# Kernel optimization log

Hardware: AMD Instinct MI355X
Metric: run time of the kernel (lower is better)

Reference implementation:

```python
import jax, jax.numpy as jnp
import numpy as np

N = 100000   # nodes
E = 1600000  # edges (before self loops)
IN, HID, HEADS, OUT = 128, 32, 2, 32


def setup_inputs() -> dict:
    key = jax.random.key(0)
    ks = jax.random.split(key, 10)
    def glorot(k, shape, fan_in):
        return jax.random.normal(k, shape, dtype=jnp.float32) / np.sqrt(fan_in)
    return {
        "x": jax.random.normal(ks[0], (N, IN), dtype=jnp.float32),
        "edge_index": jax.random.randint(ks[1], (2, E), 0, N, dtype=jnp.int32),
        "W1": glorot(ks[2], (IN, HEADS * HID), IN),
        "a_src1": glorot(ks[3], (HEADS, HID), HID),
        "a_dst1": glorot(ks[4], (HEADS, HID), HID),
        "b1": jnp.zeros((HEADS * HID,), dtype=jnp.float32),
        "W2": glorot(ks[5], (HEADS * HID, OUT), HEADS * HID),
        "a_src2": glorot(ks[6], (1, OUT), OUT),
        "a_dst2": glorot(ks[7], (1, OUT), OUT),
        "b2": jnp.zeros((OUT,), dtype=jnp.float32),
    }


def gat_conv(x, W, a_src, a_dst, b, src, dst, n):
    """PyG-style GATConv: shared linear, edge softmax over incoming edges, sum aggregate."""
    H, C = a_src.shape
    xl = (x @ W).reshape(n, H, C)                       # [N, H, C]
    asn = jnp.einsum('nhc,hc->nh', xl, a_src)            # per-node source score
    adn = jnp.einsum('nhc,hc->nh', xl, a_dst)            # per-node dest score
    e = jax.nn.leaky_relu(asn[src] + adn[dst], 0.2)      # [E', H]
    m = jax.ops.segment_max(e, dst, num_segments=n)      # stable softmax per dest
    m = jnp.where(jnp.isfinite(m), m, 0.0)
    ex = jnp.exp(e - m[dst])
    denom = jax.ops.segment_sum(ex, dst, num_segments=n)
    alpha = ex / (denom[dst] + 1e-16)                    # [E', H]
    out = jax.ops.segment_sum(xl[src] * alpha[:, :, None], dst, num_segments=n)
    return out.reshape(n, H * C) + b


def reference(x, edge_index, W1, a_src1, a_dst1, b1, W2, a_src2, a_dst2, b2):
    n = x.shape[0]
    loop = jnp.arange(n, dtype=edge_index.dtype)         # add self loops (PyG default)
    src = jnp.concatenate([edge_index[0], loop])
    dst = jnp.concatenate([edge_index[1], loop])
    h = jax.nn.relu(gat_conv(x, W1, a_src1, a_dst1, b1, src, dst, n))
    # F.dropout(p=0.5) is identity in eval mode
    return gat_conv(h, W2, a_src2, a_dst2, b2, src, dst, n)
```

## Files before the change

kernel.cpp:

```cpp
#include <hip/hip_runtime.h>
#include <hip/hip_fp16.h>


#define BS 256
#define PCHUNK 8192
#define CAPB 5632
#define GPAD 16

typedef _Float16 half8 __attribute__((ext_vector_type(8)));
typedef float f32x4 __attribute__((ext_vector_type(4)));

__global__ __launch_bounds__(BS) void k_init(int* __restrict__ gcursor, int nbuk) {
    for (int i = threadIdx.x; i < nbuk; i += BS) gcursor[i * GPAD] = i * CAPB;
}

__global__ __launch_bounds__(BS) void k_pg1(const int* __restrict__ ei, int E, int n,
                                            int* __restrict__ gcursor, int* __restrict__ ppair,
                                            const float* __restrict__ x, const float* __restrict__ W,
                                            const float* __restrict__ asrc, const float* __restrict__ adst,
                                            signed char* __restrict__ xl, float* __restrict__ scA,
                                            float* __restrict__ scD, int gC) {
    __shared__ _Float16 smem[8192];
    int tid = threadIdx.x;
    if ((int)blockIdx.x < gC) {
        int* cnt  = (int*)smem;
        int* gpos = cnt + 512;
        int* lcur = cnt + 1024;
        cnt[tid] = 0; cnt[tid + 256] = 0;
        lcur[tid] = 0; lcur[tid + 256] = 0;
        __syncthreads();
        const int* dstp = ei + E;
        int base = blockIdx.x * PCHUNK;
        bool full = (base + PCHUNK <= E);
        if (full) {
            const int4* dv = (const int4*)(dstp + base) + tid * 8;
#pragma unroll
            for (int k = 0; k < 8; k++) {
                int4 d4 = dv[k];
                atomicAdd(&cnt[d4.x >> 8], 1);
                atomicAdd(&cnt[d4.y >> 8], 1);
                atomicAdd(&cnt[d4.z >> 8], 1);
                atomicAdd(&cnt[d4.w >> 8], 1);
            }
        } else {
            for (int i = tid; base + i < E; i += BS)
                atomicAdd(&cnt[dstp[base + i] >> 8], 1);
        }
        __syncthreads();
        for (int b = tid; b < 512; b += BS) {
            int c = cnt[b];
            if (c > 0) gpos[b] = atomicAdd(&gcursor[b * GPAD], c);
        }
        __syncthreads();
        if (full) {
            const int4* sv = (const int4*)(ei + base) + tid * 8;
            const int4* dv = (const int4*)(dstp + base) + tid * 8;
#pragma unroll 2
            for (int k = 0; k < 8; k++) {
                int4 s4 = sv[k];
                int4 d4 = dv[k];
                int d, s, b, r;
                d = d4.x; s = s4.x; b = d >> 8; r = atomicAdd(&lcur[b], 1);
                ppair[gpos[b] + r] = ((d & 255) << 17) | s;
                d = d4.y; s = s4.y; b = d >> 8; r = atomicAdd(&lcur[b], 1);
                ppair[gpos[b] + r] = ((d & 255) << 17) | s;
                d = d4.z; s = s4.z; b = d >> 8; r = atomicAdd(&lcur[b], 1);
                ppair[gpos[b] + r] = ((d & 255) << 17) | s;
                d = d4.w; s = s4.w; b = d >> 8; r = atomicAdd(&lcur[b], 1);
                ppair[gpos[b] + r] = ((d & 255) << 17) | s;
            }
        } else {
            for (int i = tid; base + i < E; i += BS) {
                int s = ei[base + i], d = dstp[base + i];
                int b = d >> 8;
                int r = atomicAdd(&lcur[b], 1);
                ppair[gpos[b] + r] = ((d & 255) << 17) | s;
            }
        }
        return;
    }
    _Float16* wf = smem;
#pragma unroll
    for (int v = 0; v < 8; v++) {
        int w = (v * 256 + tid) * 4;
        float4 ww = *(const float4*)(W + w);
        int k = w >> 6, c0 = w & 63;
        int kt = k >> 5, j = k & 7, lnh = (k >> 3) & 3;
        int nt = c0 >> 4;
        int f = kt * 4 + nt;
        int bidx = (f * 64 + lnh * 16 + (c0 & 15)) * 8 + j;
        wf[bidx]      = (_Float16)ww.x;
        wf[bidx + 8]  = (_Float16)ww.y;
        wf[bidx + 16] = (_Float16)ww.z;
        wf[bidx + 24] = (_Float16)ww.w;
    }
    __syncthreads();
    int wave = tid >> 6, lane = tid & 63;
    int nb = ((blockIdx.x - gC) * 4 + wave) * 16;
    int m = lane & 15, q = lane >> 4;
    int node_m = nb + m; if (node_m >= n) node_m = n - 1;
    half8 bf[4][4];
#pragma unroll
    for (int f = 0; f < 16; f++)
        bf[f >> 2][f & 3] = *(half8*)&wf[(f * 64 + lane) * 8];
    f32x4 acc[4] = {f32x4{0,0,0,0}, f32x4{0,0,0,0}, f32x4{0,0,0,0}, f32x4{0,0,0,0}};
#pragma unroll
    for (int kt = 0; kt < 4; kt++) {
        const float* xp = x + (size_t)node_m * 128 + kt * 32 + q * 8;
        float4 xa = *(const float4*)xp;
        float4 xb = *(const float4*)(xp + 4);
        half8 a;
        a[0] = (_Float16)xa.x; a[1] = (_Float16)xa.y; a[2] = (_Float16)xa.z; a[3] = (_Float16)xa.w;
        a[4] = (_Float16)xb.x; a[5] = (_Float16)xb.y; a[6] = (_Float16)xb.z; a[7] = (_Float16)xb.w;
#pragma unroll
        for (int nt = 0; nt < 4; nt++)
            acc[nt] = __builtin_amdgcn_mfma_f32_16x16x32_f16(a, bf[kt][nt], acc[nt], 0, 0, 0);
    }
    int c = lane & 15;
    float a_s[4], a_d[4];
#pragma unroll
    for (int nt = 0; nt < 4; nt++) { a_s[nt] = asrc[nt * 16 + c]; a_d[nt] = adst[nt * 16 + c]; }
#pragma unroll
    for (int r = 0; r < 4; r++) {
        int node = nb + q * 4 + r;
        bool ok = node < n;
        float v0 = acc[0][r], v1 = acc[1][r], v2 = acc[2][r], v3 = acc[3][r];
        float as0 = v0 * a_s[0] + v1 * a_s[1];
        float as1 = v2 * a_s[2] + v3 * a_s[3];
        float ad0 = v0 * a_d[0] + v1 * a_d[1];
        float ad1 = v2 * a_d[2] + v3 * a_d[3];
        float mxv = fmaxf(fmaxf(fabsf(v0), fabsf(v1)), fmaxf(fabsf(v2), fabsf(v3)));
#pragma unroll
        for (int off = 1; off < 16; off <<= 1) {
            as0 += __shfl_xor(as0, off); as1 += __shfl_xor(as1, off);
            ad0 += __shfl_xor(ad0, off); ad1 += __shfl_xor(ad1, off);
            mxv = fmaxf(mxv, __shfl_xor(mxv, off));
        }
        if (ok) {
            float inv = mxv > 1e-30f ? 127.f / mxv : 0.f;
            float scl = mxv * (1.f / 127.f);
            signed char* row = xl + (size_t)node * 64;
            row[c]      = (signed char)(int)rintf(v0 * inv);
            row[16 + c] = (signed char)(int)rintf(v1 * inv);
            row[32 + c] = (signed char)(int)rintf(v2 * inv);
            row[48 + c] = (signed char)(int)rintf(v3 * inv);
            if (c == 0) {
                ((float4*)scA)[node] = make_float4(as0, as1, scl, 0.f);
                ((float2*)scD)[node] = make_float2(ad0, ad1);
            }
        }
    }
}

__global__ __launch_bounds__(BS) void k_bucket(const int* __restrict__ ppair,
                                               const int* __restrict__ gcursor, int n,
                                               int* __restrict__ col,
                                               int* __restrict__ row_ptr, int* __restrict__ row_end) {
    __shared__ int ldeg[256];
    __shared__ int lscan[256];
    __shared__ int lcur[256];
    __shared__ int lcol[CAPB];
    int b = blockIdx.x;
    int t = threadIdx.x;
    int lo = b << 8;
    int hi = lo + 256; if (hi > n) hi = n;
    int W = hi - lo;
    int base = b * CAPB;
    int cnt = gcursor[b * GPAD] - base;
    if (cnt > CAPB) cnt = CAPB;
    ldeg[t] = 0;
    __syncthreads();
    for (int i = t; i < cnt; i += BS)
        atomicAdd(&ldeg[ppair[base + i] >> 17], 1);
    __syncthreads();
    lscan[t] = ldeg[t];
    __syncthreads();
    for (int off = 1; off < 256; off <<= 1) {
        int a = (t >= off) ? lscan[t - off] : 0;
        __syncthreads();
        lscan[t] += a;
        __syncthreads();
    }
    {
        int e0 = lscan[t] - ldeg[t];
        lcur[t] = e0;
        if (t < W) { row_ptr[lo + t] = base + e0; row_end[lo + t] = base + e0 + ldeg[t]; }
    }
    __syncthreads();
    for (int i = t; i < cnt; i += BS) {
        int p = ppair[base + i];
        int r = atomicAdd(&lcur[p >> 17], 1);
        if (r < CAPB) lcol[r] = p & 131071;
    }
    __syncthreads();
    for (int i = t; i < cnt; i += BS) col[base + i] = lcol[i];
}

__global__ __launch_bounds__(BS) void k_ag1g2(const int* __restrict__ row_ptr, const int* __restrict__ row_end,
                                              const int* __restrict__ col, const signed char* __restrict__ xl,
                                              const float* __restrict__ scA, const float* __restrict__ scD,
                                              const float* __restrict__ b1,
                                              const float* __restrict__ W2,
                                              const float* __restrict__ as2, const float* __restrict__ ad2,
                                              __half* __restrict__ xl2, float* __restrict__ sc2, int n) {
    __shared__ _Float16 hsh[32 * 72];
    __shared__ _Float16 wf2[2048];
    int tid = threadIdx.x;
#pragma unroll
    for (int v = 0; v < 2; v++) {
        int w = (v * 256 + tid) * 4;
        float4 ww = *(const float4*)(W2 + w);
        int k = w >> 5, c0 = w & 31;
        int kt = k >> 5, j = k & 7, lnh = (k >> 3) & 3;
        int nt = c0 >> 4;
        int f = kt * 2 + nt;
        int bidx = (f * 64 + lnh * 16 + (c0 & 15)) * 8 + j;
        wf2[bidx]      = (_Float16)ww.x;
        wf2[bidx + 8]  = (_Float16)ww.y;
        wf2[bidx + 16] = (_Float16)ww.z;
        wf2[bidx + 24] = (_Float16)ww.w;
    }
    int node_local = tid >> 3;
    int node = blockIdx.x * 32 + node_local;
    int tc = tid & 7;
    int lane = tid & 63;
    int tb = lane & 56;
    bool alive = node < n;
    int nodeC = alive ? node : n - 1;
    int s0 = row_ptr[nodeC], e1 = row_end[nodeC];
    float4 sA = ((const float4*)scA)[nodeC];
    float2 sD = ((const float2*)scD)[nodeC];
    bool hh0 = tc < 4;
    float adn = hh0 ? sD.x : sD.y;
    float es0 = sA.x + sD.x; es0 = fmaxf(es0, 0.2f * es0);
    float es1 = sA.y + sD.y; es1 = fmaxf(es1, 0.2f * es1);
    float xs = __expf(hh0 ? es0 : es1);
    uint2 rawS = *(const uint2*)(xl + (size_t)nodeC * 64 + tc * 8);
    float ws0 = xs * sA.z;
    int sx = (int)rawS.x, sy = (int)rawS.y;
    float acc0 = ws0 * (float)(signed char)(sx);
    float acc1 = ws0 * (float)(signed char)(sx >> 8);
    float acc2 = ws0 * (float)(signed char)(sx >> 16);
    float acc3 = ws0 * (float)(signed char)(sx >> 24);
    float acc4 = ws0 * (float)(signed char)(sy);
    float acc5 = ws0 * (float)(signed char)(sy >> 8);
    float acc6 = ws0 * (float)(signed char)(sy >> 16);
    float acc7 = ws0 * (float)(signed char)(sy >> 24);
    float den = xs;
    int deg = e1 - s0;
    int mx = deg;
    mx = max(mx, __shfl_xor(mx, 8));
    mx = max(mx, __shfl_xor(mx, 16));
    mx = max(mx, __shfl_xor(mx, 32));
    int nch = (mx + 7) >> 3;
    for (int ci = 0; ci < nch; ci++) {
        int pos = s0 + ci * 8;
        int m = e1 - pos; m = m < 0 ? 0 : (m > 8 ? 8 : m);
        int srcv = 0; float sgx = 0.f, sgy = 0.f, sgz = 0.f;
        if (tc < m) {
            srcv = col[pos + tc];
            float4 sg = ((const float4*)scA)[srcv];
            sgx = sg.x; sgy = sg.y; sgz = sg.z;
        }
#pragma unroll
        for (int kb = 0; kb < 8; kb += 4) {
            int rem = m - kb;
            if (rem > 0) {
                int nv = rem < 4 ? rem : 4;
                uint2 rr[4];
#pragma unroll
                for (int k = 0; k < 4; k++) {
                    if (k < nv) {
                        int sE = __shfl(srcv, tb + kb + k);
                        rr[k] = *(const uint2*)(xl + (size_t)sE * 64 + tc * 8);
                    }
                }
#pragma unroll
                for (int k = 0; k < 4; k++) {
                    if (k < nv) {
                        float a0 = __shfl(sgx, tb + kb + k);
                        float a1 = __shfl(sgy, tb + kb + k);
                        float sc_ = __shfl(sgz, tb + kb + k);
                        float as_ = hh0 ? a0 : a1;
                        float e = as_ + adn; e = fmaxf(e, 0.2f * e);
                        float w = __expf(e);
                        float wq = w * sc_;
                        int wx = (int)rr[k].x, wy = (int)rr[k].y;
                        acc0 = fmaf(wq, (float)(signed char)(wx), acc0);
                        acc1 = fmaf(wq, (float)(signed char)(wx >> 8), acc1);
                        acc2 = fmaf(wq, (float)(signed char)(wx >> 16), acc2);
                        acc3 = fmaf(wq, (float)(signed char)(wx >> 24), acc3);
                        acc4 = fmaf(wq, (float)(signed char)(wy), acc4);
                        acc5 = fmaf(wq, (float)(signed char)(wy >> 8), acc5);
                        acc6 = fmaf(wq, (float)(signed char)(wy >> 16), acc6);
                        acc7 = fmaf(wq, (float)(signed char)(wy >> 24), acc7);
                        den += w;
                    }
                }
            }
        }
    }
    float dinv = 1.f / (den + 1e-16f);
    {
        float4 bvA = ((const float4*)b1)[tc * 2];
        float4 bvB = ((const float4*)b1)[tc * 2 + 1];
        __half2 p0 = __floats2half2_rn(fmaxf(fmaf(acc0, dinv, bvA.x), 0.f),
                                       fmaxf(fmaf(acc1, dinv, bvA.y), 0.f));
        __half2 p1 = __floats2half2_rn(fmaxf(fmaf(acc2, dinv, bvA.z), 0.f),
                                       fmaxf(fmaf(acc3, dinv, bvA.w), 0.f));
        __half2 p2 = __floats2half2_rn(fmaxf(fmaf(acc4, dinv, bvB.x), 0.f),
                                       fmaxf(fmaf(acc5, dinv, bvB.y), 0.f));
        __half2 p3 = __floats2half2_rn(fmaxf(fmaf(acc6, dinv, bvB.z), 0.f),
                                       fmaxf(fmaf(acc7, dinv, bvB.w), 0.f));
        uint4 o;
        o.x = *(unsigned int*)&p0; o.y = *(unsigned int*)&p1;
        o.z = *(unsigned int*)&p2; o.w = *(unsigned int*)&p3;
        *(uint4*)&hsh[node_local * 72 + tc * 8] = o;
    }
    __syncthreads();
    int wave = tid >> 6;
    if (wave < 2) {
        int m2 = lane & 15, q2 = lane >> 4;
        int nl = wave * 16 + m2;
        half8 bf[2][2];
#pragma unroll
        for (int f = 0; f < 4; f++)
            bf[f >> 1][f & 1] = *(half8*)&wf2[(f * 64 + lane) * 8];
        f32x4 acc2g[2] = {f32x4{0,0,0,0}, f32x4{0,0,0,0}};
#pragma unroll
        for (int kt = 0; kt < 2; kt++) {
            half8 a = *(half8*)&hsh[nl * 72 + kt * 32 + q2 * 8];
#pragma unroll
            for (int nt = 0; nt < 2; nt++)
                acc2g[nt] = __builtin_amdgcn_mfma_f32_16x16x32_f16(a, bf[kt][nt], acc2g[nt], 0, 0, 0);
        }
        int c = lane & 15;
        float a_s[2], a_d[2];
#pragma unroll
        for (int nt = 0; nt < 2; nt++) { a_s[nt] = as2[nt * 16 + c]; a_d[nt] = ad2[nt * 16 + c]; }
#pragma unroll
        for (int r = 0; r < 4; r++) {
            int nl_r = wave * 16 + q2 * 4 + r;
            int node_r = blockIdx.x * 32 + nl_r;
            bool ok = node_r < n;
            float v0 = acc2g[0][r], v1 = acc2g[1][r];
            float as = v0 * a_s[0] + v1 * a_s[1];
            float ad = v0 * a_d[0] + v1 * a_d[1];
#pragma unroll
            for (int off = 1; off < 16; off <<= 1) {
                as += __shfl_xor(as, off); ad += __shfl_xor(ad, off);
            }
            if (ok) {
                __half* row = xl2 + (size_t)node_r * 32;
                row[c]      = __float2half(v0);
                row[16 + c] = __float2half(v1);
                if (c == 0) ((float2*)sc2)[node_r] = make_float2(as, ad);
            }
        }
    }
}

__global__ __launch_bounds__(BS) void k_agg2(const int* __restrict__ row_ptr, const int* __restrict__ row_end,
                                             const int* __restrict__ col, const __half* __restrict__ xl,
                                             const float* __restrict__ sc, const float* __restrict__ asrc,
                                             const float* __restrict__ b2,
                                             float* __restrict__ out, int n) {
    int tid = blockIdx.x * BS + threadIdx.x;
    int node = tid >> 2;
    int tc = threadIdx.x & 3;
    int lane = threadIdx.x & 63;
    int tb = lane & 60;
    bool alive = node < n;
    if (!alive) node = n - 1;
    int s0 = row_ptr[node], e1 = row_end[node];
    float2 sn = ((const float2*)sc)[node];
    float adn = sn.y;
    float es = sn.x + adn; es = fmaxf(es, 0.2f * es);
    float xs = __expf(es);
    uint4 rawS = *(const uint4*)(xl + (size_t)node * 32 + tc * 8);
    __half2 sh0 = *(__half2*)&rawS.x, sh1 = *(__half2*)&rawS.y;
    __half2 sh2 = *(__half2*)&rawS.z, sh3 = *(__half2*)&rawS.w;
    float acc0 = xs * __low2float(sh0), acc1 = xs * __high2float(sh0);
    float acc2 = xs * __low2float(sh1), acc3 = xs * __high2float(sh1);
    float acc4 = xs * __low2float(sh2), acc5 = xs * __high2float(sh2);
    float acc6 = xs * __low2float(sh3), acc7 = xs * __high2float(sh3);
    float den = xs;
    int deg = e1 - s0;
    int mx = deg;
    mx = max(mx, __shfl_xor(mx, 4));
    mx = max(mx, __shfl_xor(mx, 8));
    mx = max(mx, __shfl_xor(mx, 16));
    mx = max(mx, __shfl_xor(mx, 32));
    int nch = (mx + 3) >> 2;
    for (int ci = 0; ci < nch; ci++) {
        int pos = s0 + ci * 4;
        int m = e1 - pos; m = m < 0 ? 0 : (m > 4 ? 4 : m);
        int srcv = 0; float sA = 0.f;
        if (tc < m) {
            srcv = col[pos + tc];
            sA = sc[(size_t)srcv * 2];
        }
        if (m > 0) {
            uint4 rr[4];
#pragma unroll
            for (int k = 0; k < 4; k++) {
                if (k < m) {
                    int sE = __shfl(srcv, tb + k);
                    rr[k] = *(const uint4*)(xl + (size_t)sE * 32 + tc * 8);
                }
            }
#pragma unroll
            for (int k = 0; k < 4; k++) {
                if (k < m) {
                    float s = __shfl(sA, tb + k);
                    float e = s + adn; e = fmaxf(e, 0.2f * e);
                    float w = __expf(e);
                    __half2 q0 = *(__half2*)&rr[k].x, q1 = *(__half2*)&rr[k].y;
                    __half2 q2 = *(__half2*)&rr[k].z, q3 = *(__half2*)&rr[k].w;
                    acc0 = fmaf(w, __low2float(q0), acc0); acc1 = fmaf(w, __high2float(q0), acc1);
                    acc2 = fmaf(w, __low2float(q1), acc2); acc3 = fmaf(w, __high2float(q1), acc3);
                    acc4 = fmaf(w, __low2float(q2), acc4); acc5 = fmaf(w, __high2float(q2), acc5);
                    acc6 = fmaf(w, __low2float(q3), acc6); acc7 = fmaf(w, __high2float(q3), acc7);
                    den += w;
                }
            }
        }
    }
    float dinv = 1.f / (den + 1e-16f);
    if (alive) {
        float4 bvA = ((const float4*)b2)[tc * 2];
        float4 bvB = ((const float4*)b2)[tc * 2 + 1];
        float4 oA, oB;
        oA.x = fmaf(acc0, dinv, bvA.x);
        oA.y = fmaf(acc1, dinv, bvA.y);
        oA.z = fmaf(acc2, dinv, bvA.z);
        oA.w = fmaf(acc3, dinv, bvA.w);
        oB.x = fmaf(acc4, dinv, bvB.x);
        oB.y = fmaf(acc5, dinv, bvB.y);
        oB.z = fmaf(acc6, dinv, bvB.z);
        oB.w = fmaf(acc7, dinv, bvB.w);
        float4* orow = (float4*)(out + (size_t)node * 32);
        orow[tc * 2]     = oA;
        orow[tc * 2 + 1] = oB;
    }
}

extern "C" void kernel_launch(void* const* d_in, const int* in_sizes, int n_in,
                              void* d_out, int out_size, void* d_ws, size_t ws_size,
                              hipStream_t stream) {
    const float* x    = (const float*)d_in[0];
    const int*   ei   = (const int*)d_in[1];
    const float* W1   = (const float*)d_in[2];
    const float* as1  = (const float*)d_in[3];
    const float* ad1  = (const float*)d_in[4];
    const float* b1   = (const float*)d_in[5];
    const float* W2   = (const float*)d_in[6];
    const float* as2  = (const float*)d_in[7];
    const float* ad2  = (const float*)d_in[8];
    const float* b2   = (const float*)d_in[9];
    int n = in_sizes[0] / 128;
    int E = in_sizes[1] / 2;
    int NBUK = (n + 255) >> 8;

    char* w = (char*)d_ws;
    auto alloc = [&](size_t bytes) -> char* {
        char* p = w; w += (bytes + 255) / 256 * 256; return p;
    };
    int*    gcursor = (int*)alloc((size_t)NBUK * GPAD * 4);
    int*    ppair   = (int*)alloc((size_t)NBUK * CAPB * 4);
    int*    col     = (int*)alloc((size_t)NBUK * CAPB * 4);
    int*    row_ptr = (int*)alloc((size_t)n * 4);
    int*    row_end = (int*)alloc((size_t)n * 4);
    signed char* xl1 = (signed char*)alloc((size_t)n * 64);
    float*  scA     = (float*)alloc((size_t)n * 4 * 4);
    float*  scD     = (float*)alloc((size_t)n * 2 * 4);
    __half* xl2     = (__half*)alloc((size_t)n * 32 * 2);
    float*  sc2     = (float*)alloc((size_t)n * 2 * 4);

    int gC  = (E + PCHUNK - 1) / PCHUNK;
    int gG  = (n + 63) / 64;
    int gA1 = (n * 8 + BS - 1) / BS;
    int gA2 = (n * 4 + BS - 1) / BS;

    k_init   <<<1, BS, 0, stream>>>(gcursor, NBUK);
    k_pg1    <<<gC + gG, BS, 0, stream>>>(ei, E, n, gcursor, ppair,
                                          x, W1, as1, ad1, xl1, scA, scD, gC);
    k_bucket <<<NBUK, BS, 0, stream>>>(ppair, gcursor, n, col, row_ptr, row_end);
    k_ag1g2  <<<gA1, BS, 0, stream>>>(row_ptr, row_end, col, xl1, scA, scD, b1,
                                      W2, as2, ad2, xl2, sc2, n);
    k_agg2   <<<gA2, BS, 0, stream>>>(row_ptr, row_end, col, xl2, sc2, as2, b2,
                                      (float*)d_out, n);
}
```

Baseline: 211.3 us.

## Move layer-1 GEMM from partition kernel into bucket-sort kernel, 256 nodes per block

The layer-1 feature transform (x@W1 via MFMA, int8 quantization, attention scores) is taken out of the edge-partition kernel and fused into the per-bucket CSR build kernel as extra blocks. The partition kernel now runs alone with small shared memory, which should raise its occupancy. GEMM blocks now process 256 nodes each (4 tiles per wave), so W is converted to fp16 in LDS once per 256 nodes instead of once per 64. The catch is that the bucket kernel's large LDS footprint now also applies to the GEMM blocks, and the GEMM no longer overlaps with the atomic-heavy partition phase.

```diff
diff --git a/kernel.cpp b/kernel.cpp
--- a/kernel.cpp
+++ b/kernel.cpp
@@ -14,72 +14,118 @@
     for (int i = threadIdx.x; i < nbuk; i += BS) gcursor[i * GPAD] = i * CAPB;
 }
 
-__global__ __launch_bounds__(BS) void k_pg1(const int* __restrict__ ei, int E, int n,
-                                            int* __restrict__ gcursor, int* __restrict__ ppair,
-                                            const float* __restrict__ x, const float* __restrict__ W,
-                                            const float* __restrict__ asrc, const float* __restrict__ adst,
-                                            signed char* __restrict__ xl, float* __restrict__ scA,
-                                            float* __restrict__ scD, int gC) {
-    __shared__ _Float16 smem[8192];
+__global__ __launch_bounds__(BS) void k_part(const int* __restrict__ ei, int E, int n,
+                                             int* __restrict__ gcursor, int* __restrict__ ppair) {
+    __shared__ int smem[1536];
     int tid = threadIdx.x;
-    if ((int)blockIdx.x < gC) {
-        int* cnt  = (int*)smem;
-        int* gpos = cnt + 512;
-        int* lcur = cnt + 1024;
-        cnt[tid] = 0; cnt[tid + 256] = 0;
-        lcur[tid] = 0; lcur[tid + 256] = 0;
+    int* cnt  = smem;
+    int* gpos = cnt + 512;
+    int* lcur = cnt + 1024;
+    cnt[tid] = 0; cnt[tid + 256] = 0;
+    lcur[tid] = 0; lcur[tid + 256] = 0;
+    __syncthreads();
+    const int* dstp = ei + E;
+    int base = blockIdx.x * PCHUNK;
+    bool full = (base + PCHUNK <= E);
+    if (full) {
+        const int4* dv = (const int4*)(dstp + base) + tid * 8;
+#pragma unroll
+        for (int k = 0; k < 8; k++) {
+            int4 d4 = dv[k];
+            atomicAdd(&cnt[d4.x >> 8], 1);
+            atomicAdd(&cnt[d4.y >> 8], 1);
+            atomicAdd(&cnt[d4.z >> 8], 1);
+            atomicAdd(&cnt[d4.w >> 8], 1);
+        }
+    } else {
+        for (int i = tid; base + i < E; i += BS)
+            atomicAdd(&cnt[dstp[base + i] >> 8], 1);
+    }
+    __syncthreads();
+    for (int b = tid; b < 512; b += BS) {
+        int c = cnt[b];
+        if (c > 0) gpos[b] = atomicAdd(&gcursor[b * GPAD], c);
+    }
+    __syncthreads();
+    if (full) {
+        const int4* sv = (const int4*)(ei + base) + tid * 8;
+        const int4* dv = (const int4*)(dstp + base) + tid * 8;
+#pragma unroll 2
+        for (int k = 0; k < 8; k++) {
+            int4 s4 = sv[k];
+            int4 d4 = dv[k];
+            int d, s, b, r;
+            d = d4.x; s = s4.x; b = d >> 8; r = atomicAdd(&lcur[b], 1);
+            ppair[gpos[b] + r] = ((d & 255) << 17) | s;
+            d = d4.y; s = s4.y; b = d >> 8; r = atomicAdd(&lcur[b], 1);
+            ppair[gpos[b] + r] = ((d & 255) << 17) | s;
+            d = d4.z; s = s4.z; b = d >> 8; r = atomicAdd(&lcur[b], 1);
+            ppair[gpos[b] + r] = ((d & 255) << 17) | s;
+            d = d4.w; s = s4.w; b = d >> 8; r = atomicAdd(&lcur[b], 1);
+            ppair[gpos[b] + r] = ((d & 255) << 17) | s;
+        }
+    } else {
+        for (int i = tid; base + i < E; i += BS) {
+            int s = ei[base + i], d = dstp[base + i];
+            int b = d >> 8;
+            int r = atomicAdd(&lcur[b], 1);
+            ppair[gpos[b] + r] = ((d & 255) << 17) | s;
+        }
+    }
+}
+
+__global__ __launch_bounds__(BS) void k_g1bkt(const int* __restrict__ ppair,
+                                              const int* __restrict__ gcursor, int n, int nbk,
+                                              int* __restrict__ col,
+                                              int* __restrict__ row_ptr, int* __restrict__ row_end,
+                                              const float* __restrict__ x, const float* __restrict__ W,
+                                              const float* __restrict__ asrc, const float* __restrict__ adst,
+                                              signed char* __restrict__ xl, float* __restrict__ scA,
+                                              float* __restrict__ scD) {
+    __shared__ int smem4[6400];
+    int tid = threadIdx.x;
+    if ((int)blockIdx.x < nbk) {
+        int* ldeg  = smem4;
+        int* lscan = smem4 + 256;
+        int* lcur  = smem4 + 512;
+        int* lcol  = smem4 + 768;
+        int b = blockIdx.x;
+        int t = tid;
+        int lo = b << 8;
+        int hi = lo + 256; if (hi > n) hi = n;
+        int Wd = hi - lo;
+        int base = b * CAPB;
+        int cnt = gcursor[b * GPAD] - base;
+        if (cnt > CAPB) cnt = CAPB;
+        ldeg[t] = 0;
         __syncthreads();
-        const int* dstp = ei + E;
-        int base = blockIdx.x * PCHUNK;
-        bool full = (base + PCHUNK <= E);
-        if (full) {
-            const int4* dv = (const int4*)(dstp + base) + tid * 8;
-#pragma unroll
-            for (int k = 0; k < 8; k++) {
-                int4 d4 = dv[k];
-                atomicAdd(&cnt[d4.x >> 8], 1);
-                atomicAdd(&cnt[d4.y >> 8], 1);
-                atomicAdd(&cnt[d4.z >> 8], 1);
-                atomicAdd(&cnt[d4.w >> 8], 1);
-            }
-        } else {
-            for (int i = tid; base + i < E; i += BS)
-                atomicAdd(&cnt[dstp[base + i] >> 8], 1);
-        }
+        for (int i = t; i < cnt; i += BS)
+            atomicAdd(&ldeg[ppair[base + i] >> 17], 1);
         __syncthreads();
-        for (int b = tid; b < 512; b += BS) {
-            int c = cnt[b];
-            if (c > 0) gpos[b] = atomicAdd(&gcursor[b * GPAD], c);
-        }
+        lscan[t] = ldeg[t];
         __syncthreads();
-        if (full) {
-            const int4* sv = (const int4*)(ei + base) + tid * 8;
-            const int4* dv = (const int4*)(dstp + base) + tid * 8;
-#pragma unroll 2
-            for (int k = 0; k < 8; k++) {
-                int4 s4 = sv[k];
-                int4 d4 = dv[k];
-                int d, s, b, r;
-                d = d4.x; s = s4.x; b = d >> 8; r = atomicAdd(&lcur[b], 1);
-                ppair[gpos[b] + r] = ((d & 255) << 17) | s;
-                d = d4.y; s = s4.y; b = d >> 8; r = atomicAdd(&lcur[b], 1);
-                ppair[gpos[b] + r] = ((d & 255) << 17) | s;
-                d = d4.z; s = s4.z; b = d >> 8; r = atomicAdd(&lcur[b], 1);
-                ppair[gpos[b] + r] = ((d & 255) << 17) | s;
-                d = d4.w; s = s4.w; b = d >> 8; r = atomicAdd(&lcur[b], 1);
-                ppair[gpos[b] + r] = ((d & 255) << 17) | s;
-            }
-        } else {
-            for (int i = tid; base + i < E; i += BS) {
-                int s = ei[base + i], d = dstp[base + i];
-                int b = d >> 8;
-                int r = atomicAdd(&lcur[b], 1);
-                ppair[gpos[b] + r] = ((d & 255) << 17) | s;
-            }
-        }
+        for (int off = 1; off < 256; off <<= 1) {
+            int a = (t >= off) ? lscan[t - off] : 0;
+            __syncthreads();
+            lscan[t] += a;
+            __syncthreads();
+        }
+        {
+            int e0 = lscan[t] - ldeg[t];
+            lcur[t] = e0;
+            if (t < Wd) { row_ptr[lo + t] = base + e0; row_end[lo + t] = base + e0 + ldeg[t]; }
+        }
+        __syncthreads();
+        for (int i = t; i < cnt; i += BS) {
+            int p = ppair[base + i];
+            int r = atomicAdd(&lcur[p >> 17], 1);
+            if (r < CAPB) lcol[r] = p & 131071;
+        }
+        __syncthreads();
+        for (int i = t; i < cnt; i += BS) col[base + i] = lcol[i];
         return;
     }
-    _Float16* wf = smem;
+    _Float16* wf = (_Float16*)smem4;
 #pragma unroll
     for (int v = 0; v < 8; v++) {
         int w = (v * 256 + tid) * 4;
@@ -96,104 +142,64 @@
     }
     __syncthreads();
     int wave = tid >> 6, lane = tid & 63;
-    int nb = ((blockIdx.x - gC) * 4 + wave) * 16;
     int m = lane & 15, q = lane >> 4;
-    int node_m = nb + m; if (node_m >= n) node_m = n - 1;
-    half8 bf[4][4];
-#pragma unroll
-    for (int f = 0; f < 16; f++)
-        bf[f >> 2][f & 3] = *(half8*)&wf[(f * 64 + lane) * 8];
-    f32x4 acc[4] = {f32x4{0,0,0,0}, f32x4{0,0,0,0}, f32x4{0,0,0,0}, f32x4{0,0,0,0}};
-#pragma unroll
-    for (int kt = 0; kt < 4; kt++) {
-        const float* xp = x + (size_t)node_m * 128 + kt * 32 + q * 8;
-        float4 xa = *(const float4*)xp;
-        float4 xb = *(const float4*)(xp + 4);
-        half8 a;
-        a[0] = (_Float16)xa.x; a[1] = (_Float16)xa.y; a[2] = (_Float16)xa.z; a[3] = (_Float16)xa.w;
-        a[4] = (_Float16)xb.x; a[5] = (_Float16)xb.y; a[6] = (_Float16)xb.z; a[7] = (_Float16)xb.w;
-#pragma unroll
-        for (int nt = 0; nt < 4; nt++)
-            acc[nt] = __builtin_amdgcn_mfma_f32_16x16x32_f16(a, bf[kt][nt], acc[nt], 0, 0, 0);
-    }
     int c = lane & 15;
     float a_s[4], a_d[4];
 #pragma unroll
     for (int nt = 0; nt < 4; nt++) { a_s[nt] = asrc[nt * 16 + c]; a_d[nt] = adst[nt * 16 + c]; }
-#pragma unroll
-    for (int r = 0; r < 4; r++) {
-        int node = nb + q * 4 + r;
-        bool ok = node < n;
-        float v0 = acc[0][r], v1 = acc[1][r], v2 = acc[2][r], v3 = acc[3][r];
-        float as0 = v0 * a_s[0] + v1 * a_s[1];
-        float as1 = v2 * a_s[2] + v3 * a_s[3];
-        float ad0 = v0 * a_d[0] + v1 * a_d[1];
-        float ad1 = v2 * a_d[2] + v3 * a_d[3];
-        float mxv = fmaxf(fmaxf(fabsf(v0), fabsf(v1)), fmaxf(fabsf(v2), fabsf(v3)));
-#pragma unroll
-        for (int off = 1; off < 16; off <<= 1) {
-            as0 += __shfl_xor(as0, off); as1 += __shfl_xor(as1, off);
-            ad0 += __shfl_xor(ad0, off); ad1 += __shfl_xor(ad1, off);
-            mxv = fmaxf(mxv, __shfl_xor(mxv, off));
-        }
-        if (ok) {
-            float inv = mxv > 1e-30f ? 127.f / mxv : 0.f;
-            float scl = mxv * (1.f / 127.f);
-            signed char* row = xl + (size_t)node * 64;
-            row[c]      = (signed char)(int)rintf(v0 * inv);
-            row[16 + c] = (signed char)(int)rintf(v1 * inv);
-            row[32 + c] = (signed char)(int)rintf(v2 * inv);
-            row[48 + c] = (signed char)(int)rintf(v3 * inv);
-            if (c == 0) {
-                ((float4*)scA)[node] = make_float4(as0, as1, scl, 0.f);
-                ((float2*)scD)[node] = make_float2(ad0, ad1);
-            }
-        }
-    }
-}
-
-__global__ __launch_bounds__(BS) void k_bucket(const int* __restrict__ ppair,
-                                               const int* __restrict__ gcursor, int n,
-                                               int* __restrict__ col,
-                                               int* __restrict__ row_ptr, int* __restrict__ row_end) {
-    __shared__ int ldeg[256];
-    __shared__ int lscan[256];
-    __shared__ int lcur[256];
-    __shared__ int lcol[CAPB];
-    int b = blockIdx.x;
-    int t = threadIdx.x;
-    int lo = b << 8;
-    int hi = lo + 256; if (hi > n) hi = n;
-    int W = hi - lo;
-    int base = b * CAPB;
-    int cnt = gcursor[b * GPAD] - base;
-    if (cnt > CAPB) cnt = CAPB;
-    ldeg[t] = 0;
-    __syncthreads();
-    for (int i = t; i < cnt; i += BS)
-        atomicAdd(&ldeg[ppair[base + i] >> 17], 1);
-    __syncthreads();
-    lscan[t] = ldeg[t];
-    __syncthreads();
-    for (int off = 1; off < 256; off <<= 1) {
-        int a = (t >= off) ? lscan[t - off] : 0;
-        __syncthreads();
-        lscan[t] += a;
-        __syncthreads();
-    }
-    {
-        int e0 = lscan[t] - ldeg[t];
-        lcur[t] = e0;
-        if (t < W) { row_ptr[lo + t] = base + e0; row_end[lo + t] = base + e0 + ldeg[t]; }
-    }
-    __syncthreads();
-    for (int i = t; i < cnt; i += BS) {
-        int p = ppair[base + i];
-        int r = atomicAdd(&lcur[p >> 17], 1);
-        if (r < CAPB) lcol[r] = p & 131071;
-    }
-    __syncthreads();
-    for (int i = t; i < cnt; i += BS) col[base + i] = lcol[i];
+    int base256 = ((int)blockIdx.x - nbk) * 256 + wave * 64;
+#pragma unroll
+    for (int t = 0; t < 4; t++) {
+        int nb = base256 + t * 16;
+        int node_m = nb + m; if (node_m >= n) node_m = n - 1;
+        half8 bf[4][4];
+#pragma unroll
+        for (int f = 0; f < 16; f++)
+            bf[f >> 2][f & 3] = *(half8*)&wf[(f * 64 + lane) * 8];
+        f32x4 acc[4] = {f32x4{0,0,0,0}, f32x4{0,0,0,0}, f32x4{0,0,0,0}, f32x4{0,0,0,0}};
+#pragma unroll
+        for (int kt = 0; kt < 4; kt++) {
+            const float* xp = x + (size_t)node_m * 128 + kt * 32 + q * 8;
+            float4 xa = *(const float4*)xp;
+            float4 xb = *(const float4*)(xp + 4);
+            half8 a;
+            a[0] = (_Float16)xa.x; a[1] = (_Float16)xa.y; a[2] = (_Float16)xa.z; a[3] = (_Float16)xa.w;
+            a[4] = (_Float16)xb.x; a[5] = (_Float16)xb.y; a[6] = (_Float16)xb.z; a[7] = (_Float16)xb.w;
+#pragma unroll
+            for (int nt = 0; nt < 4; nt++)
+                acc[nt] = __builtin_amdgcn_mfma_f32_16x16x32_f16(a, bf[kt][nt], acc[nt], 0, 0, 0);
+        }
+#pragma unroll
+        for (int r = 0; r < 4; r++) {
+            int node = nb + q * 4 + r;
+            bool ok = node < n;
+            float v0 = acc[0][r], v1 = acc[1][r], v2 = acc[2][r], v3 = acc[3][r];
+            float as0 = v0 * a_s[0] + v1 * a_s[1];
+            float as1 = v2 * a_s[2] + v3 * a_s[3];
+            float ad0 = v0 * a_d[0] + v1 * a_d[1];
+            float ad1 = v2 * a_d[2] + v3 * a_d[3];
+            float mxv = fmaxf(fmaxf(fabsf(v0), fabsf(v1)), fmaxf(fabsf(v2), fabsf(v3)));
+#pragma unroll
+            for (int off = 1; off < 16; off <<= 1) {
+                as0 += __shfl_xor(as0, off); as1 += __shfl_xor(as1, off);
+                ad0 += __shfl_xor(ad0, off); ad1 += __shfl_xor(ad1, off);
+                mxv = fmaxf(mxv, __shfl_xor(mxv, off));
+            }
+            if (ok) {
+                float inv = mxv > 1e-30f ? 127.f / mxv : 0.f;
+                float scl = mxv * (1.f / 127.f);
+                signed char* row = xl + (size_t)node * 64;
+                row[c]      = (signed char)(int)rintf(v0 * inv);
+                row[16 + c] = (signed char)(int)rintf(v1 * inv);
+                row[32 + c] = (signed char)(int)rintf(v2 * inv);
+                row[48 + c] = (signed char)(int)rintf(v3 * inv);
+                if (c == 0) {
+                    ((float4*)scA)[node] = make_float4(as0, as1, scl, 0.f);
+                    ((float2*)scD)[node] = make_float2(ad0, ad1);
+                }
+            }
+        }
+    }
 }
 
 __global__ __launch_bounds__(BS) void k_ag1g2(const int* __restrict__ row_ptr, const int* __restrict__ row_end,
@@ -478,14 +484,15 @@
     float*  sc2     = (float*)alloc((size_t)n * 2 * 4);
 
     int gC  = (E + PCHUNK - 1) / PCHUNK;
-    int gG  = (n + 63) / 64;
+    int gG1 = (n + 255) / 256;
     int gA1 = (n * 8 + BS - 1) / BS;
     int gA2 = (n * 4 + BS - 1) / BS;
 
     k_init   <<<1, BS, 0, stream>>>(gcursor, NBUK);
-    k_pg1    <<<gC + gG, BS, 0, stream>>>(ei, E, n, gcursor, ppair,
-                                          x, W1, as1, ad1, xl1, scA, scD, gC);
-    k_bucket <<<NBUK, BS, 0, stream>>>(ppair, gcursor, n, col, row_ptr, row_end);
+    k_part   <<<gC, BS, 0, stream>>>(ei, E, n, gcursor, ppair);
+    k_g1bkt  <<<NBUK + gG1, BS, 0, stream>>>(ppair, gcursor, n, NBUK,
+                                             col, row_ptr, row_end,
+                                             x, W1, as1, ad1, xl1, scA, scD);
     k_ag1g2  <<<gA1, BS, 0, stream>>>(row_ptr, row_end, col, xl1, scA, scD, b1,
                                       W2, as2, ad2, xl2, sc2, n);
     k_agg2   <<<gA2, BS, 0, stream>>>(row_ptr, row_end, col, xl2, sc2, as2, b2,
```

After: 205.4 us. -2.8%, faster.
